# Kernel tuning notes

Hardware: AMD Instinct MI355X
Metric: run time of the kernel (lower is better)

Reference implementation:

```python
import jax, jax.numpy as jnp
import numpy as np

U, I, D = 100000, 150000, 64
N = U + I
E = 1250000
KEEP_RATE = 0.8


def setup_inputs() -> dict:
    key = jax.random.key(0)
    k1, k2, k3, k4, k5, k6 = jax.random.split(key, 6)
    row = jax.random.randint(k1, (E,), 0, N, dtype=jnp.int32)
    col = jax.random.randint(k2, (E,), 0, N, dtype=jnp.int32)
    adj_values = jax.random.uniform(k3, (E,), dtype=jnp.float32)
    # edge dropout mask: floor(rand + keep_rate) in {0,1}, exactly as SpAdjEdgeDrop
    edge_mask = jnp.floor(jax.random.uniform(k4, (E,), dtype=jnp.float32) + KEEP_RATE)
    user_embeds = jax.random.normal(k5, (U, D), dtype=jnp.float32)
    item_embeds = jax.random.normal(k6, (I, D), dtype=jnp.float32)
    return {
        "row": row,
        "col": col,
        "adj_values": adj_values,
        "edge_mask": edge_mask,
        "user_embeds": user_embeds,
        "item_embeds": item_embeds,
        "layer_num": 3,
    }


def reference(row, col, adj_values, edge_mask, user_embeds, item_embeds, layer_num):
    user_num = user_embeds.shape[0]
    n_nodes = user_num + item_embeds.shape[0]
    # edge-dropped sparse values (mask==0 edges contribute nothing to spmm)
    vals = adj_values * edge_mask  # [E]
    embeds = jnp.concatenate([user_embeds, item_embeds], axis=0)  # [N, D]
    acc = embeds
    cur = embeds
    for _ in range(layer_num):
        # spmm: out[r] += vals[e] * cur[c] for each edge e=(r,c)
        msgs = vals[:, None] * cur[col]  # [E, D] gather
        cur = jax.ops.segment_sum(msgs, row, num_segments=n_nodes)  # [N, D] scatter-add
        acc = acc + cur
    out = acc / (layer_num + 1)
    return out[:user_num], out[user_num:]
```

## Files before the change

### kernel.cpp

```cpp
#include <hip/hip_runtime.h>


#define U_NODES 100000
#define N_NODES 250000
#define DIM4 16
#define E_EDGES 1250000
#define SCAN_TILE 1024
#define NBUCKET 32

typedef unsigned short u16;

__device__ __forceinline__ u16 f2bf(float f) {
    unsigned u = __float_as_uint(f);
    u += 0x7fffu + ((u >> 16) & 1u);
    return (u16)(u >> 16);
}
__device__ __forceinline__ float blo(unsigned u) {
    return __uint_as_float(u << 16);
}
__device__ __forceinline__ float bhi(unsigned u) {
    return __uint_as_float(u & 0xffff0000u);
}
__device__ __forceinline__ int4 gat16(const u16* __restrict__ base, int node, int part) {
    return ((const int4*)(base + ((size_t)node << 6)))[part];
}
__device__ __forceinline__ void fma8(float4& sa, float4& sb, float v, int4 h) {
    sa.x += v * blo((unsigned)h.x);
    sa.y += v * bhi((unsigned)h.x);
    sa.z += v * blo((unsigned)h.y);
    sa.w += v * bhi((unsigned)h.y);
    sb.x += v * blo((unsigned)h.z);
    sb.y += v * bhi((unsigned)h.z);
    sb.z += v * blo((unsigned)h.w);
    sb.w += v * bhi((unsigned)h.w);
}

__global__ void lgcn_convert(const float4* __restrict__ user4,
                             const float4* __restrict__ item4,
                             u16* __restrict__ e0b) {
    long i = (long)blockIdx.x * blockDim.x + threadIdx.x;
    const long total = (long)N_NODES * DIM4;
    if (i >= total) return;
    const long uc = (long)U_NODES * DIM4;
    float4 v = (i < uc) ? user4[i] : item4[i - uc];
    ((ushort4*)e0b)[i] = make_ushort4(f2bf(v.x), f2bf(v.y), f2bf(v.z), f2bf(v.w));
}

__global__ void lgcn_count(const int* __restrict__ row,
                           const float* __restrict__ mask,
                           int* __restrict__ counts,
                           int* __restrict__ epos) {
    int e = blockIdx.x * blockDim.x + threadIdx.x;
    if (e >= E_EDGES) return;
    if (mask[e] != 0.0f) epos[e] = atomicAdd(&counts[row[e]], 1);
}

__global__ void lgcn_offsets(const int* __restrict__ counts,
                             int2* __restrict__ rowdesc,
                             int* __restrict__ total,
                             int* __restrict__ bcount,
                             int* __restrict__ rowpos) {
    __shared__ int lds[256];
    __shared__ int sbase;
    __shared__ int lbc[NBUCKET];
    __shared__ int lbb[NBUCKET];
    int t = threadIdx.x;
    if (t < NBUCKET) lbc[t] = 0;
    __syncthreads();
    int base = blockIdx.x * SCAN_TILE + t * 4;
    int4 c = make_int4(0, 0, 0, 0);
    if (base + 3 < N_NODES) {
        c = *(const int4*)(counts + base);
    } else {
        if (base + 0 < N_NODES) c.x = counts[base + 0];
        if (base + 1 < N_NODES) c.y = counts[base + 1];
        if (base + 2 < N_NODES) c.z = counts[base + 2];
        if (base + 3 < N_NODES) c.w = counts[base + 3];
    }
    int4 p = make_int4((c.x + 3) & ~3, (c.y + 3) & ~3, (c.z + 3) & ~3, (c.w + 3) & ~3);
    int s = p.x + p.y + p.z + p.w;
    int b0 = (c.x + 3) >> 2; if (b0 > NBUCKET - 1) b0 = NBUCKET - 1;
    int b1 = (c.y + 3) >> 2; if (b1 > NBUCKET - 1) b1 = NBUCKET - 1;
    int b2 = (c.z + 3) >> 2; if (b2 > NBUCKET - 1) b2 = NBUCKET - 1;
    int b3 = (c.w + 3) >> 2; if (b3 > NBUCKET - 1) b3 = NBUCKET - 1;
    int l0 = 0, l1 = 0, l2 = 0, l3 = 0;
    if (base + 0 < N_NODES) l0 = atomicAdd(&lbc[b0], 1);
    if (base + 1 < N_NODES) l1 = atomicAdd(&lbc[b1], 1);
    if (base + 2 < N_NODES) l2 = atomicAdd(&lbc[b2], 1);
    if (base + 3 < N_NODES) l3 = atomicAdd(&lbc[b3], 1);
    lds[t] = s;
    __syncthreads();
    if (t < NBUCKET) lbb[t] = atomicAdd(&bcount[t], lbc[t]);
    for (int off = 1; off < 256; off <<= 1) {
        int v = (t >= off) ? lds[t - off] : 0;
        __syncthreads();
        if (t >= off) lds[t] += v;
        __syncthreads();
    }
    if (t == 255) sbase = atomicAdd(total, lds[255]);
    __syncthreads();
    int pos = sbase + lds[t] - s;
    if (base + 0 < N_NODES) { rowdesc[base + 0] = make_int2(pos, c.x); rowpos[base + 0] = ((lbb[b0] + l0) << 5) | b0; } pos += p.x;
    if (base + 1 < N_NODES) { rowdesc[base + 1] = make_int2(pos, c.y); rowpos[base + 1] = ((lbb[b1] + l1) << 5) | b1; } pos += p.y;
    if (base + 2 < N_NODES) { rowdesc[base + 2] = make_int2(pos, c.z); rowpos[base + 2] = ((lbb[b2] + l2) << 5) | b2; } pos += p.z;
    if (base + 3 < N_NODES) { rowdesc[base + 3] = make_int2(pos, c.w); rowpos[base + 3] = ((lbb[b3] + l3) << 5) | b3; }
}

__global__ void lgcn_perm(const int* __restrict__ bcount,
                          const int* __restrict__ rowpos,
                          const int2* __restrict__ rowdesc,
                          int4* __restrict__ permdesc) {
    __shared__ int bb[NBUCKET];
    int t = threadIdx.x;
    if (t == 0) {
        int s = 0;
        for (int i = NBUCKET - 1; i >= 0; --i) { bb[i] = s; s += bcount[i]; }
    }
    __syncthreads();
    int r = blockIdx.x * blockDim.x + t;
    if (r >= N_NODES) return;
    int pk = rowpos[r];
    int2 rd = rowdesc[r];
    permdesc[bb[pk & 31] + (pk >> 5)] = make_int4(rd.x, rd.y, r, 0);
}

__global__ void lgcn_fill(const int* __restrict__ row,
                          const int* __restrict__ col,
                          const float* __restrict__ adj,
                          const float* __restrict__ mask,
                          const int2* __restrict__ rowdesc,
                          const int* __restrict__ epos,
                          int2* __restrict__ csr) {
    int e = blockIdx.x * blockDim.x + threadIdx.x;
    if (e >= E_EDGES) return;
    float m = mask[e];
    if (m == 0.0f) return;
    int2 rd = rowdesc[row[e]];
    int rank = epos[e];
    csr[rd.x + rank] = make_int2(col[e], __float_as_int(adj[e] * m));
    if (rank == rd.y - 1) {
        int pe = (rd.y + 3) & ~3;
        for (int p = rd.y; p < pe; ++p) csr[rd.x + p] = make_int2(0, 0);
    }
}

template <bool LAST>
__global__ void lgcn_pull(const int4* __restrict__ permdesc,
                          const int2* __restrict__ csr,
                          const u16*  __restrict__ curb,
                          const u16*  __restrict__ e0b,
                          const u16*  __restrict__ e1b,
                          u16*        __restrict__ outb,
                          float4*     __restrict__ out) {
    int tid = blockIdx.x * blockDim.x + threadIdx.x;
    int g = tid >> 3;
    if (g >= N_NODES) return;
    int part = tid & 7;
    int4 d = permdesc[g];
    int start = d.x;
    int pend  = start + ((d.y + 3) & ~3);
    float4 sa = make_float4(0.f, 0.f, 0.f, 0.f);
    float4 sb = make_float4(0.f, 0.f, 0.f, 0.f);
    int e = start;
    for (; e + 8 <= pend; e += 8) {
        int4 ca = *(const int4*)(csr + e);
        int4 cb = *(const int4*)(csr + e + 2);
        int4 cc = *(const int4*)(csr + e + 4);
        int4 cd = *(const int4*)(csr + e + 6);
        int4 h0 = gat16(curb, ca.x, part);
        int4 h1 = gat16(curb, ca.z, part);
        int4 h2 = gat16(curb, cb.x, part);
        int4 h3 = gat16(curb, cb.z, part);
        int4 h4 = gat16(curb, cc.x, part);
        int4 h5 = gat16(curb, cc.z, part);
        int4 h6 = gat16(curb, cd.x, part);
        int4 h7 = gat16(curb, cd.z, part);
        fma8(sa, sb, __int_as_float(ca.y), h0);
        fma8(sa, sb, __int_as_float(ca.w), h1);
        fma8(sa, sb, __int_as_float(cb.y), h2);
        fma8(sa, sb, __int_as_float(cb.w), h3);
        fma8(sa, sb, __int_as_float(cc.y), h4);
        fma8(sa, sb, __int_as_float(cc.w), h5);
        fma8(sa, sb, __int_as_float(cd.y), h6);
        fma8(sa, sb, __int_as_float(cd.w), h7);
    }
    if (e < pend) {
        int4 ca = *(const int4*)(csr + e);
        int4 cb = *(const int4*)(csr + e + 2);
        int4 h0 = gat16(curb, ca.x, part);
        int4 h1 = gat16(curb, ca.z, part);
        int4 h2 = gat16(curb, cb.x, part);
        int4 h3 = gat16(curb, cb.z, part);
        fma8(sa, sb, __int_as_float(ca.y), h0);
        fma8(sa, sb, __int_as_float(ca.w), h1);
        fma8(sa, sb, __int_as_float(cb.y), h2);
        fma8(sa, sb, __int_as_float(cb.w), h3);
    }
    int r = d.z;
    size_t oi = (size_t)r * 8 + part;
    if (LAST) {
        int4 a0 = ((const int4*)e0b)[oi];
        int4 a1 = ((const int4*)e1b)[oi];
        int4 a2 = ((const int4*)curb)[oi];
        float4 o0, o1;
        o0.x = (sa.x + blo((unsigned)a0.x) + blo((unsigned)a1.x) + blo((unsigned)a2.x)) * 0.25f;
        o0.y = (sa.y + bhi((unsigned)a0.x) + bhi((unsigned)a1.x) + bhi((unsigned)a2.x)) * 0.25f;
        o0.z = (sa.z + blo((unsigned)a0.y) + blo((unsigned)a1.y) + blo((unsigned)a2.y)) * 0.25f;
        o0.w = (sa.w + bhi((unsigned)a0.y) + bhi((unsigned)a1.y) + bhi((unsigned)a2.y)) * 0.25f;
        o1.x = (sb.x + blo((unsigned)a0.z) + blo((unsigned)a1.z) + blo((unsigned)a2.z)) * 0.25f;
        o1.y = (sb.y + bhi((unsigned)a0.z) + bhi((unsigned)a1.z) + bhi((unsigned)a2.z)) * 0.25f;
        o1.z = (sb.z + blo((unsigned)a0.w) + blo((unsigned)a1.w) + blo((unsigned)a2.w)) * 0.25f;
        o1.w = (sb.w + bhi((unsigned)a0.w) + bhi((unsigned)a1.w) + bhi((unsigned)a2.w)) * 0.25f;
        out[(size_t)r * 16 + part * 2]     = o0;
        out[(size_t)r * 16 + part * 2 + 1] = o1;
    } else {
        unsigned p0 = (unsigned)f2bf(sa.x) | ((unsigned)f2bf(sa.y) << 16);
        unsigned p1 = (unsigned)f2bf(sa.z) | ((unsigned)f2bf(sa.w) << 16);
        unsigned p2 = (unsigned)f2bf(sb.x) | ((unsigned)f2bf(sb.y) << 16);
        unsigned p3 = (unsigned)f2bf(sb.z) | ((unsigned)f2bf(sb.w) << 16);
        ((int4*)outb)[oi] = make_int4((int)p0, (int)p1, (int)p2, (int)p3);
    }
}

extern "C" void kernel_launch(void* const* d_in, const int* in_sizes, int n_in,
                              void* d_out, int out_size, void* d_ws, size_t ws_size,
                              hipStream_t stream) {
    const int*   row  = (const int*)d_in[0];
    const int*   col  = (const int*)d_in[1];
    const float* adj  = (const float*)d_in[2];
    const float* mask = (const float*)d_in[3];
    const float4* user4 = (const float4*)d_in[4];
    const float4* item4 = (const float4*)d_in[5];

    float4* acc = (float4*)d_out;

    const size_t bemb_bytes = (size_t)N_NODES * 64 * sizeof(u16);
    char* p = (char*)d_ws;
    u16* e0b = (u16*)p;  p += bemb_bytes;
    u16* e1b = (u16*)p;  p += bemb_bytes;
    u16* e2b = (u16*)p;  p += bemb_bytes;
    int* total  = (int*)p;
    int* bcount = (int*)(p + 64);
    int* counts = (int*)(p + 256);
    p += 256 + (((size_t)N_NODES * 4 + 63) & ~63ul);
    int2* rowdesc  = (int2*)p;  p += ((size_t)N_NODES * 8 + 63) & ~63ul;
    int*  rowpos   = (int*)p;   p += ((size_t)N_NODES * 4 + 63) & ~63ul;
    int*  epos     = (int*)p;   p += ((size_t)E_EDGES * 4 + 63) & ~63ul;
    int4* permdesc = (int4*)p;  p += ((size_t)N_NODES * 16 + 63) & ~63ul;
    int2* csr      = (int2*)p;

    const int BLK = 256;
    const long node_vec4 = (long)N_NODES * DIM4;
    const int  grid_conv = (int)((node_vec4 + BLK - 1) / BLK);
    const int  grid_edge = (E_EDGES + BLK - 1) / BLK;
    const int  nblk_scan = (N_NODES + SCAN_TILE - 1) / SCAN_TILE;
    const int  grid_perm = (N_NODES + BLK - 1) / BLK;
    const long pull_thr  = (long)N_NODES * 8;
    const int  grid_pull = (int)((pull_thr + BLK - 1) / BLK);

    hipMemsetAsync(total, 0, 256 + (size_t)N_NODES * sizeof(int), stream);
    lgcn_convert<<<grid_conv, BLK, 0, stream>>>(user4, item4, e0b);
    lgcn_count<<<grid_edge, BLK, 0, stream>>>(row, mask, counts, epos);
    lgcn_offsets<<<nblk_scan, BLK, 0, stream>>>(counts, rowdesc, total, bcount, rowpos);
    lgcn_perm<<<grid_perm, BLK, 0, stream>>>(bcount, rowpos, rowdesc, permdesc);
    lgcn_fill<<<grid_edge, BLK, 0, stream>>>(row, col, adj, mask, rowdesc, epos, csr);

    lgcn_pull<false><<<grid_pull, BLK, 0, stream>>>(permdesc, csr, e0b, nullptr, nullptr, e1b, nullptr);
    lgcn_pull<false><<<grid_pull, BLK, 0, stream>>>(permdesc, csr, e1b, nullptr, nullptr, e2b, nullptr);
    lgcn_pull<true ><<<grid_pull, BLK, 0, stream>>>(permdesc, csr, e2b, e0b, e1b, nullptr, acc);
}
```

Before: 326.3 us.

## Fold row permutation into offsets kernel, pack descriptors, use nontemporal stores

The separate permutation kernel is removed: each scan tile now sorts its rows by degree bucket locally and writes a packed 8-byte descriptor (start offset, degree<<18 | row id) straight into the permuted slot. This drops a kernel launch, the global bucket counters and the rowpos array, and halves descriptor reads in the three pull passes. Sorting is now only within each 1024-row tile rather than global, so load balance across waves may be a little worse. It also vectorises the bf16 conversion to 8 floats per thread and uses nontemporal stores for the pull outputs.

```diff
diff --git a/kernel.cpp b/kernel.cpp
--- a/kernel.cpp
+++ b/kernel.cpp
@@ -3,17 +3,18 @@
 
 #define U_NODES 100000
 #define N_NODES 250000
-#define DIM4 16
 #define E_EDGES 1250000
 #define SCAN_TILE 1024
 #define NBUCKET 32
 
 typedef unsigned short u16;
-
-__device__ __forceinline__ u16 f2bf(float f) {
+typedef float __attribute__((ext_vector_type(4))) f32x4;
+typedef int   __attribute__((ext_vector_type(4))) i32x4;
+
+__device__ __forceinline__ unsigned f2bf(float f) {
     unsigned u = __float_as_uint(f);
     u += 0x7fffu + ((u >> 16) & 1u);
-    return (u16)(u >> 16);
+    return u >> 16;
 }
 __device__ __forceinline__ float blo(unsigned u) {
     return __uint_as_float(u << 16);
@@ -34,16 +35,31 @@
     sb.z += v * blo((unsigned)h.w);
     sb.w += v * bhi((unsigned)h.w);
 }
+__device__ __forceinline__ void nts_f4(float4 v, float4* p) {
+    f32x4 t; t.x = v.x; t.y = v.y; t.z = v.z; t.w = v.w;
+    __builtin_nontemporal_store(t, (f32x4*)p);
+}
+__device__ __forceinline__ void nts_i4(int4 v, int4* p) {
+    i32x4 t; t.x = v.x; t.y = v.y; t.z = v.z; t.w = v.w;
+    __builtin_nontemporal_store(t, (i32x4*)p);
+}
 
 __global__ void lgcn_convert(const float4* __restrict__ user4,
                              const float4* __restrict__ item4,
                              u16* __restrict__ e0b) {
     long i = (long)blockIdx.x * blockDim.x + threadIdx.x;
-    const long total = (long)N_NODES * DIM4;
+    const long total = (long)N_NODES * 8;
     if (i >= total) return;
-    const long uc = (long)U_NODES * DIM4;
-    float4 v = (i < uc) ? user4[i] : item4[i - uc];
-    ((ushort4*)e0b)[i] = make_ushort4(f2bf(v.x), f2bf(v.y), f2bf(v.z), f2bf(v.w));
+    const long uc = (long)U_NODES * 8;
+    const float4* src = (i < uc) ? (user4 + 2 * i) : (item4 + 2 * (i - uc));
+    float4 a = src[0];
+    float4 b = src[1];
+    int4 o;
+    o.x = (int)(f2bf(a.x) | (f2bf(a.y) << 16));
+    o.y = (int)(f2bf(a.z) | (f2bf(a.w) << 16));
+    o.z = (int)(f2bf(b.x) | (f2bf(b.y) << 16));
+    o.w = (int)(f2bf(b.z) | (f2bf(b.w) << 16));
+    ((int4*)e0b)[i] = o;
 }
 
 __global__ void lgcn_count(const int* __restrict__ row,
@@ -58,12 +74,11 @@
 __global__ void lgcn_offsets(const int* __restrict__ counts,
                              int2* __restrict__ rowdesc,
                              int* __restrict__ total,
-                             int* __restrict__ bcount,
-                             int* __restrict__ rowpos) {
+                             int2* __restrict__ permdesc) {
     __shared__ int lds[256];
     __shared__ int sbase;
     __shared__ int lbc[NBUCKET];
-    __shared__ int lbb[NBUCKET];
+    __shared__ int bpre[NBUCKET];
     int t = threadIdx.x;
     if (t < NBUCKET) lbc[t] = 0;
     __syncthreads();
@@ -79,10 +94,10 @@
     }
     int4 p = make_int4((c.x + 3) & ~3, (c.y + 3) & ~3, (c.z + 3) & ~3, (c.w + 3) & ~3);
     int s = p.x + p.y + p.z + p.w;
-    int b0 = (c.x + 3) >> 2; if (b0 > NBUCKET - 1) b0 = NBUCKET - 1;
-    int b1 = (c.y + 3) >> 2; if (b1 > NBUCKET - 1) b1 = NBUCKET - 1;
-    int b2 = (c.z + 3) >> 2; if (b2 > NBUCKET - 1) b2 = NBUCKET - 1;
-    int b3 = (c.w + 3) >> 2; if (b3 > NBUCKET - 1) b3 = NBUCKET - 1;
+    int b0 = p.x >> 2; if (b0 > NBUCKET - 1) b0 = NBUCKET - 1;
+    int b1 = p.y >> 2; if (b1 > NBUCKET - 1) b1 = NBUCKET - 1;
+    int b2 = p.z >> 2; if (b2 > NBUCKET - 1) b2 = NBUCKET - 1;
+    int b3 = p.w >> 2; if (b3 > NBUCKET - 1) b3 = NBUCKET - 1;
     int l0 = 0, l1 = 0, l2 = 0, l3 = 0;
     if (base + 0 < N_NODES) l0 = atomicAdd(&lbc[b0], 1);
     if (base + 1 < N_NODES) l1 = atomicAdd(&lbc[b1], 1);
@@ -90,7 +105,10 @@
     if (base + 3 < N_NODES) l3 = atomicAdd(&lbc[b3], 1);
     lds[t] = s;
     __syncthreads();
-    if (t < NBUCKET) lbb[t] = atomicAdd(&bcount[t], lbc[t]);
+    if (t == 0) {
+        int acc = 0;
+        for (int i = NBUCKET - 1; i >= 0; --i) { bpre[i] = acc; acc += lbc[i]; }
+    }
     for (int off = 1; off < 256; off <<= 1) {
         int v = (t >= off) ? lds[t - off] : 0;
         __syncthreads();
@@ -100,28 +118,11 @@
     if (t == 255) sbase = atomicAdd(total, lds[255]);
     __syncthreads();
     int pos = sbase + lds[t] - s;
-    if (base + 0 < N_NODES) { rowdesc[base + 0] = make_int2(pos, c.x); rowpos[base + 0] = ((lbb[b0] + l0) << 5) | b0; } pos += p.x;
-    if (base + 1 < N_NODES) { rowdesc[base + 1] = make_int2(pos, c.y); rowpos[base + 1] = ((lbb[b1] + l1) << 5) | b1; } pos += p.y;
-    if (base + 2 < N_NODES) { rowdesc[base + 2] = make_int2(pos, c.z); rowpos[base + 2] = ((lbb[b2] + l2) << 5) | b2; } pos += p.z;
-    if (base + 3 < N_NODES) { rowdesc[base + 3] = make_int2(pos, c.w); rowpos[base + 3] = ((lbb[b3] + l3) << 5) | b3; }
-}
-
-__global__ void lgcn_perm(const int* __restrict__ bcount,
-                          const int* __restrict__ rowpos,
-                          const int2* __restrict__ rowdesc,
-                          int4* __restrict__ permdesc) {
-    __shared__ int bb[NBUCKET];
-    int t = threadIdx.x;
-    if (t == 0) {
-        int s = 0;
-        for (int i = NBUCKET - 1; i >= 0; --i) { bb[i] = s; s += bcount[i]; }
-    }
-    __syncthreads();
-    int r = blockIdx.x * blockDim.x + t;
-    if (r >= N_NODES) return;
-    int pk = rowpos[r];
-    int2 rd = rowdesc[r];
-    permdesc[bb[pk & 31] + (pk >> 5)] = make_int4(rd.x, rd.y, r, 0);
+    int tb = blockIdx.x * SCAN_TILE;
+    if (base + 0 < N_NODES) { rowdesc[base + 0] = make_int2(pos, c.x); permdesc[tb + bpre[b0] + l0] = make_int2(pos, (c.x << 18) | (base + 0)); } pos += p.x;
+    if (base + 1 < N_NODES) { rowdesc[base + 1] = make_int2(pos, c.y); permdesc[tb + bpre[b1] + l1] = make_int2(pos, (c.y << 18) | (base + 1)); } pos += p.y;
+    if (base + 2 < N_NODES) { rowdesc[base + 2] = make_int2(pos, c.z); permdesc[tb + bpre[b2] + l2] = make_int2(pos, (c.z << 18) | (base + 2)); } pos += p.z;
+    if (base + 3 < N_NODES) { rowdesc[base + 3] = make_int2(pos, c.w); permdesc[tb + bpre[b3] + l3] = make_int2(pos, (c.w << 18) | (base + 3)); }
 }
 
 __global__ void lgcn_fill(const int* __restrict__ row,
@@ -145,7 +146,7 @@
 }
 
 template <bool LAST>
-__global__ void lgcn_pull(const int4* __restrict__ permdesc,
+__global__ void lgcn_pull(const int2* __restrict__ permdesc,
                           const int2* __restrict__ csr,
                           const u16*  __restrict__ curb,
                           const u16*  __restrict__ e0b,
@@ -156,9 +157,10 @@
     int g = tid >> 3;
     if (g >= N_NODES) return;
     int part = tid & 7;
-    int4 d = permdesc[g];
+    int2 d = permdesc[g];
     int start = d.x;
-    int pend  = start + ((d.y + 3) & ~3);
+    int pk = d.y;
+    int pend = start + (((pk >> 18) + 3) & ~3);
     float4 sa = make_float4(0.f, 0.f, 0.f, 0.f);
     float4 sb = make_float4(0.f, 0.f, 0.f, 0.f);
     int e = start;
@@ -196,7 +198,7 @@
         fma8(sa, sb, __int_as_float(cb.y), h2);
         fma8(sa, sb, __int_as_float(cb.w), h3);
     }
-    int r = d.z;
+    int r = pk & 0x3ffff;
     size_t oi = (size_t)r * 8 + part;
     if (LAST) {
         int4 a0 = ((const int4*)e0b)[oi];
@@ -211,14 +213,15 @@
         o1.y = (sb.y + bhi((unsigned)a0.z) + bhi((unsigned)a1.z) + bhi((unsigned)a2.z)) * 0.25f;
         o1.z = (sb.z + blo((unsigned)a0.w) + blo((unsigned)a1.w) + blo((unsigned)a2.w)) * 0.25f;
         o1.w = (sb.w + bhi((unsigned)a0.w) + bhi((unsigned)a1.w) + bhi((unsigned)a2.w)) * 0.25f;
-        out[(size_t)r * 16 + part * 2]     = o0;
-        out[(size_t)r * 16 + part * 2 + 1] = o1;
+        nts_f4(o0, &out[(size_t)r * 16 + part * 2]);
+        nts_f4(o1, &out[(size_t)r * 16 + part * 2 + 1]);
     } else {
-        unsigned p0 = (unsigned)f2bf(sa.x) | ((unsigned)f2bf(sa.y) << 16);
-        unsigned p1 = (unsigned)f2bf(sa.z) | ((unsigned)f2bf(sa.w) << 16);
-        unsigned p2 = (unsigned)f2bf(sb.x) | ((unsigned)f2bf(sb.y) << 16);
-        unsigned p3 = (unsigned)f2bf(sb.z) | ((unsigned)f2bf(sb.w) << 16);
-        ((int4*)outb)[oi] = make_int4((int)p0, (int)p1, (int)p2, (int)p3);
+        int4 o;
+        o.x = (int)(f2bf(sa.x) | (f2bf(sa.y) << 16));
+        o.y = (int)(f2bf(sa.z) | (f2bf(sa.w) << 16));
+        o.z = (int)(f2bf(sb.x) | (f2bf(sb.y) << 16));
+        o.w = (int)(f2bf(sb.z) | (f2bf(sb.w) << 16));
+        nts_i4(o, &((int4*)outb)[oi]);
     }
 }
 
@@ -240,29 +243,25 @@
     u16* e1b = (u16*)p;  p += bemb_bytes;
     u16* e2b = (u16*)p;  p += bemb_bytes;
     int* total  = (int*)p;
-    int* bcount = (int*)(p + 64);
-    int* counts = (int*)(p + 256);
-    p += 256 + (((size_t)N_NODES * 4 + 63) & ~63ul);
+    int* counts = (int*)(p + 64);
+    p += 64 + (((size_t)N_NODES * 4 + 63) & ~63ul);
     int2* rowdesc  = (int2*)p;  p += ((size_t)N_NODES * 8 + 63) & ~63ul;
-    int*  rowpos   = (int*)p;   p += ((size_t)N_NODES * 4 + 63) & ~63ul;
+    int2* permdesc = (int2*)p;  p += ((size_t)N_NODES * 8 + 63) & ~63ul;
     int*  epos     = (int*)p;   p += ((size_t)E_EDGES * 4 + 63) & ~63ul;
-    int4* permdesc = (int4*)p;  p += ((size_t)N_NODES * 16 + 63) & ~63ul;
     int2* csr      = (int2*)p;
 
     const int BLK = 256;
-    const long node_vec4 = (long)N_NODES * DIM4;
-    const int  grid_conv = (int)((node_vec4 + BLK - 1) / BLK);
+    const long conv_thr  = (long)N_NODES * 8;
+    const int  grid_conv = (int)((conv_thr + BLK - 1) / BLK);
     const int  grid_edge = (E_EDGES + BLK - 1) / BLK;
     const int  nblk_scan = (N_NODES + SCAN_TILE - 1) / SCAN_TILE;
-    const int  grid_perm = (N_NODES + BLK - 1) / BLK;
     const long pull_thr  = (long)N_NODES * 8;
     const int  grid_pull = (int)((pull_thr + BLK - 1) / BLK);
 
-    hipMemsetAsync(total, 0, 256 + (size_t)N_NODES * sizeof(int), stream);
+    hipMemsetAsync(total, 0, 64 + (size_t)N_NODES * sizeof(int), stream);
     lgcn_convert<<<grid_conv, BLK, 0, stream>>>(user4, item4, e0b);
     lgcn_count<<<grid_edge, BLK, 0, stream>>>(row, mask, counts, epos);
-    lgcn_offsets<<<nblk_scan, BLK, 0, stream>>>(counts, rowdesc, total, bcount, rowpos);
-    lgcn_perm<<<grid_perm, BLK, 0, stream>>>(bcount, rowpos, rowdesc, permdesc);
+    lgcn_offsets<<<nblk_scan, BLK, 0, stream>>>(counts, rowdesc, total, permdesc);
     lgcn_fill<<<grid_edge, BLK, 0, stream>>>(row, col, adj, mask, rowdesc, epos, csr);
 
     lgcn_pull<false><<<grid_pull, BLK, 0, stream>>>(permdesc, csr, e0b, nullptr, nullptr, e1b, nullptr);
```

Result: slower. 337.2 us (+3.3%).
